# Performance work log

Hardware: AMD Instinct MI355X
Metric: run time of the kernel (lower is better)

## Reference

```python
import jax, jax.numpy as jnp
import numpy as np

B, D, H, W, C = 8, 4, 56, 56, 128
HEADS = 4
WD, WH, WW = 2, 7, 7
SD, SH, SW = 1, 3, 3
N = WD * WH * WW            # tokens per window = 98
NW = (D // WD) * (H // WH) * (W // WW)  # windows per sample = 128
SCALE = (C // HEADS) ** -0.5
EPS = 1e-5


def _rel_pos_index():
    coords = np.stack(np.meshgrid(np.arange(WD), np.arange(WH), np.arange(WW), indexing='ij'))
    coords = coords.reshape(3, -1)                    # (3, N)
    rel = (coords[:, :, None] - coords[:, None, :]).transpose(1, 2, 0)  # (N, N, 3)
    rel[:, :, 0] += WD - 1
    rel[:, :, 1] += WH - 1
    rel[:, :, 2] += WW - 1
    rel[:, :, 0] *= (2 * WH - 1) * (2 * WW - 1)
    rel[:, :, 1] *= (2 * WW - 1)
    return rel.sum(-1)                                # (N, N) int

REL_IDX = jnp.asarray(_rel_pos_index())


def _np_window_partition(x, wd, wh, ww):
    b, d, h, w, c = x.shape
    x = x.reshape(b, d // wd, wd, h // wh, wh, w // ww, ww, c)
    return x.transpose(0, 1, 3, 5, 2, 4, 6, 7).reshape(-1, wd * wh * ww, c)


def _attn_mask():
    img = np.zeros((1, D, H, W, 1), np.float32)
    cnt = 0
    for ds in (slice(None, -WD), slice(-WD, -SD), slice(-SD, None)):
        for hs in (slice(None, -WH), slice(-WH, -SH), slice(-SH, None)):
            for ws in (slice(None, -WW), slice(-WW, -SW), slice(-SW, None)):
                img[:, ds, hs, ws, :] = cnt
                cnt += 1
    mw = _np_window_partition(img, WD, WH, WW)[..., 0]         # (nW, N)
    m = mw[:, None, :] - mw[:, :, None]                        # (nW, N, N)
    return jnp.asarray(np.where(m != 0, -100.0, 0.0).astype(np.float32))

ATTN_MASK = _attn_mask()  # (nW, N, N)


def window_partition(x):
    b = x.shape[0]
    x = x.reshape(b, D // WD, WD, H // WH, WH, W // WW, WW, C)
    return x.transpose(0, 1, 3, 5, 2, 4, 6, 7).reshape(-1, N, C)


def window_reverse(wins, b):
    x = wins.reshape(b, D // WD, H // WH, W // WW, WD, WH, WW, C)
    return x.transpose(0, 1, 4, 2, 5, 3, 6, 7).reshape(b, D, H, W, C)


def layernorm(x, g, b):
    mu = jnp.mean(x, axis=-1, keepdims=True)
    var = jnp.mean(jnp.square(x - mu), axis=-1, keepdims=True)
    return (x - mu) / jnp.sqrt(var + EPS) * g + b


def swin_block(x, norm1_g, norm1_b, qkv_w, qkv_b, rpb_table, proj_w, proj_b,
               norm2_g, norm2_b, fc1_w, fc1_b, fc2_w, fc2_b):
    shortcut = x
    h1 = layernorm(x, norm1_g, norm1_b)
    # cyclic shift (pad amounts are 0 for these dims)
    shifted = jnp.roll(h1, (-SD, -SH, -SW), axis=(1, 2, 3))
    xw = window_partition(shifted)                    # (B*nW, N, C)
    Bn = xw.shape[0]
    qkv = (xw @ qkv_w + qkv_b).reshape(Bn, N, 3, HEADS, C // HEADS)
    qkv = qkv.transpose(2, 0, 3, 1, 4)                # (3, Bn, h, N, c)
    q, k, v = qkv[0], qkv[1], qkv[2]
    attn = jnp.einsum('bhnc,bhmc->bhnm', q * SCALE, k)
    bias = rpb_table[REL_IDX].transpose(2, 0, 1)      # (h, N, N)
    attn = attn + bias[None]
    attn = attn.reshape(B, NW, HEADS, N, N) + ATTN_MASK[None, :, None]
    attn = jax.nn.softmax(attn.reshape(Bn, HEADS, N, N), axis=-1)
    out = jnp.einsum('bhnm,bhmc->bhnc', attn, v)
    out = out.transpose(0, 2, 1, 3).reshape(Bn, N, C)
    out = out @ proj_w + proj_b
    xr = window_reverse(out, B)
    xr = jnp.roll(xr, (SD, SH, SW), axis=(1, 2, 3))
    x1 = shortcut + xr
    h2 = layernorm(x1, norm2_g, norm2_b)
    mlp = jax.nn.gelu(h2 @ fc1_w + fc1_b, approximate=False) @ fc2_w + fc2_b
    return x1 + mlp


def setup_inputs() -> dict:
    key = jax.random.key(0)
    ks = jax.random.split(key, 6)
    s = 0.02
    return {
        'x': jax.random.normal(ks[0], (B, D, H, W, C), jnp.float32),
        'norm1_g': jnp.ones((C,), jnp.float32),
        'norm1_b': jnp.zeros((C,), jnp.float32),
        'qkv_w': jax.random.normal(ks[1], (C, 3 * C), jnp.float32) * s,
        'qkv_b': jnp.zeros((3 * C,), jnp.float32),
        'rpb_table': jax.random.normal(ks[2], ((2 * WD - 1) * (2 * WH - 1) * (2 * WW - 1), HEADS), jnp.float32) * s,
        'proj_w': jax.random.normal(ks[3], (C, C), jnp.float32) * s,
        'proj_b': jnp.zeros((C,), jnp.float32),
        'norm2_g': jnp.ones((C,), jnp.float32),
        'norm2_b': jnp.zeros((C,), jnp.float32),
        'fc1_w': jax.random.normal(ks[4], (C, 4 * C), jnp.float32) * s,
        'fc1_b': jnp.zeros((4 * C,), jnp.float32),
        'fc2_w': jax.random.normal(ks[5], (4 * C, C), jnp.float32) * s,
        'fc2_b': jnp.zeros((C,), jnp.float32),
    }


def reference(x, norm1_g, norm1_b, qkv_w, qkv_b, rpb_table, proj_w, proj_b,
              norm2_g, norm2_b, fc1_w, fc1_b, fc2_w, fc2_b):
    return swin_block(x, norm1_g, norm1_b, qkv_w, qkv_b, rpb_table, proj_w, proj_b,
                      norm2_g, norm2_b, fc1_w, fc1_b, fc2_w, fc2_b)
```

## Files before the change

### kernel.cpp

```cpp
#include <hip/hip_runtime.h>
#include <hip/hip_bf16.h>
#include <cstdint>
#include <cstddef>

using bf16 = __hip_bfloat16;
typedef __bf16 bf16x8 __attribute__((ext_vector_type(8)));
typedef float f32x4 __attribute__((ext_vector_type(4)));

#define DEV static __device__ __forceinline__

DEV bf16 f2b(float x) { return __float2bfloat16(x); }
DEV f32x4 mfma16(bf16x8 a, bf16x8 b, f32x4 c) {
    return __builtin_amdgcn_mfma_f32_16x16x32_bf16(a, b, c, 0, 0, 0);
}
DEV float gelu_f(float x) {
    float u2 = x * x;
    float u = x * (0.7978845608028654f + 0.0356774081363001f * u2);
    float s = 1.f / (1.f + __expf(-2.f * u));
    return x * s;
}
DEV void gload16(const bf16* g, bf16* l) {
    __builtin_amdgcn_global_load_lds(
        (const __attribute__((address_space(1))) unsigned int*)g,
        (__attribute__((address_space(3))) unsigned int*)l, 16, 0, 0);
}

constexpr int NTOK = 98;
constexpr int BNWIN = 1024;
constexpr int MTOT = BNWIN * NTOK;
constexpr float SCALE = 0.17677669529663687f;
constexpr float EPS = 1e-5f;

__global__ __launch_bounds__(256) void k_prep(const float* __restrict__ qkv_w,
        const float* __restrict__ proj_w, const float* __restrict__ fc1_w,
        const float* __restrict__ fc2_w, const float* __restrict__ rpb,
        bf16* __restrict__ QW, bf16* __restrict__ PW,
        bf16* __restrict__ W1, bf16* __restrict__ W2, float* __restrict__ BT) {
    int tid = blockIdx.x * 256 + threadIdx.x;
    int stride = gridDim.x * 256;
    for (int i = tid; i < 384 * 128; i += stride) {
        int n = i >> 7, k = i & 127;
        QW[i] = f2b(qkv_w[k * 384 + n]);
    }
    for (int i = tid; i < 128 * 128; i += stride) {
        int n = i >> 7, k = i & 127;
        PW[i] = f2b(proj_w[k * 128 + n]);
    }
    for (int i = tid; i < 512 * 128; i += stride) {
        int t = i >> 13, r = (i >> 7) & 63, kswz = i & 127;
        int k = kswz ^ ((r & 7) << 3);
        W1[i] = f2b(fc1_w[(size_t)k * 512 + t * 64 + r]);
    }
    for (int i = tid; i < 512 * 128; i += stride) {
        int t = i >> 13, c = (i >> 6) & 127, kswz = i & 63;
        int kk = kswz ^ ((c & 7) << 3);
        W2[i] = f2b(fc2_w[(size_t)(t * 64 + kk) * 128 + c]);
    }
    for (int i = tid; i < 4 * 98 * 98; i += stride) {
        int h = i / 9604, r = i - h * 9604;
        int ii = r / 98, jj = r - ii * 98;
        int di = ii >= 49, ri = ii - di * 49, hi = ri / 7, wi = ri - hi * 7;
        int dj = jj >= 49, rj = jj - dj * 49, hj = rj / 7, wj = rj - hj * 7;
        int bidx = (di - dj + 1) * 169 + (hi - hj + 6) * 13 + (wi - wj + 6);
        BT[i] = rpb[bidx * 4 + h];
    }
}

__global__ __launch_bounds__(256) void k_ln1(const float* __restrict__ x,
        const float* __restrict__ g, const float* __restrict__ be,
        bf16* __restrict__ xw) {
    int wave = threadIdx.x >> 6, lane = threadIdx.x & 63;
    int r = blockIdx.x * 4 + wave;
    int bn = r / 98, n = r - bn * 98;
    int b = bn >> 7, wr = bn & 127;
    int dB = wr >> 6, hB = (wr >> 3) & 7, wB = wr & 7;
    int dd = (n >= 49), rem = n - dd * 49;
    int hh = rem / 7, ww = rem - hh * 7;
    int dp = dB * 2 + dd, hp = hB * 7 + hh, wp = wB * 7 + ww;
    int ds = (dp + 1) & 3;
    int hs = hp + 3; if (hs >= 56) hs -= 56;
    int wsv = wp + 3; if (wsv >= 56) wsv -= 56;
    size_t src = ((size_t)((b * 4 + ds) * 56 + hs) * 56 + wsv) * 128;

    float2 v = *(const float2*)&x[src + lane * 2];
    float v0 = v.x, v1 = v.y;
    float s = v0 + v1, sq = v0 * v0 + v1 * v1;
    #pragma unroll
    for (int m = 1; m < 64; m <<= 1) { s += __shfl_xor(s, m); sq += __shfl_xor(sq, m); }
    float mean = s * (1.f / 128.f);
    float var = sq * (1.f / 128.f) - mean * mean;
    float rstd = rsqrtf(var + EPS);
    float g0 = g[lane * 2], g1 = g[lane * 2 + 1];
    float e0 = be[lane * 2], e1 = be[lane * 2 + 1];
    union { uint32_t u32; bf16 h[2]; } o;
    o.h[0] = f2b((v0 - mean) * rstd * g0 + e0);
    o.h[1] = f2b((v1 - mean) * rstd * g1 + e1);
    *(uint32_t*)&xw[(size_t)r * 128 + lane * 2] = o.u32;
}

__global__ __launch_bounds__(256) void k_qkv(const bf16* __restrict__ A,
        const bf16* __restrict__ QW, const float* __restrict__ bias,
        bf16* __restrict__ out) {
    __shared__ __align__(16) bf16 As[64 * 136];
    __shared__ __align__(16) bf16 Bt[64 * 136];
    int tid = threadIdx.x;
    int row0 = blockIdx.x * 64;
    int col0 = blockIdx.y * 64;
    #pragma unroll
    for (int p = 0; p < 4; ++p) {
        int vi = tid + p * 256;
        int row = vi >> 4, cg = vi & 15;
        *(uint4*)&As[row * 136 + cg * 8] =
            *(const uint4*)&A[(size_t)(row0 + row) * 128 + cg * 8];
    }
    #pragma unroll
    for (int p = 0; p < 4; ++p) {
        int vi = tid + p * 256;
        int row = vi >> 4, cg = vi & 15;
        *(uint4*)&Bt[row * 136 + cg * 8] =
            *(const uint4*)&QW[(size_t)(col0 + row) * 128 + cg * 8];
    }
    __syncthreads();
    int wave = tid >> 6, lane = tid & 63;
    int wr = (wave >> 1) * 32, wc = (wave & 1) * 32;
    int lrow = lane & 15, kg8 = (lane >> 4) * 8, g4 = (lane >> 4) * 4;
    f32x4 acc[2][2] = {};
    #pragma unroll
    for (int ksi = 0; ksi < 4; ++ksi) {
        bf16x8 a[2], bb[2];
        #pragma unroll
        for (int t = 0; t < 2; ++t)
            a[t] = *(const bf16x8*)&As[(wr + t * 16 + lrow) * 136 + ksi * 32 + kg8];
        #pragma unroll
        for (int u2 = 0; u2 < 2; ++u2)
            bb[u2] = *(const bf16x8*)&Bt[(wc + u2 * 16 + lrow) * 136 + ksi * 32 + kg8];
        #pragma unroll
        for (int t = 0; t < 2; ++t)
            #pragma unroll
            for (int u2 = 0; u2 < 2; ++u2)
                acc[t][u2] = mfma16(a[t], bb[u2], acc[t][u2]);
    }
    #pragma unroll
    for (int t = 0; t < 2; ++t)
        #pragma unroll
        for (int u2 = 0; u2 < 2; ++u2) {
            int gcol = col0 + wc + u2 * 16 + lrow;
            float bv = bias[gcol];
            #pragma unroll
            for (int r2 = 0; r2 < 4; ++r2) {
                int grow = row0 + wr + t * 16 + g4 + r2;
                out[(size_t)grow * 384 + gcol] = f2b(acc[t][u2][r2] + bv);
            }
        }
}

__global__ __launch_bounds__(256) void k_attn(const bf16* __restrict__ qkv,
        const float* __restrict__ BT, bf16* __restrict__ aout) {
    __shared__ __align__(16) bf16 qs[112 * 40];
    __shared__ __align__(16) bf16 ksm[112 * 40];
    __shared__ __align__(16) bf16 vt[32 * 136];
    __shared__ __align__(16) bf16 ps[64 * 136];
    __shared__ signed char trg[112];

    int tid = threadIdx.x;
    int bn = blockIdx.x, h = blockIdx.y;
    int wrw = bn & 127;
    int dB = wrw >> 6, hB = (wrw >> 3) & 7, wB = wrw & 7;

    {
        uint32_t* z1 = (uint32_t*)qs;
        uint32_t* z2 = (uint32_t*)ksm;
        for (int i = tid; i < 2240; i += 256) { z1[i] = 0u; z2[i] = 0u; }
        uint32_t* z3 = (uint32_t*)vt;
        for (int i = tid; i < 2176; i += 256) z3[i] = 0u;
        uint32_t* z4 = (uint32_t*)ps;
        for (int i = tid; i < 4352; i += 256) z4[i] = 0u;
    }
    if (tid < 112) {
        int n = tid < 98 ? tid : 97;
        int dd = n >= 49, rem = n - dd * 49;
        int hh = rem / 7, ww2 = rem - hh * 7;
        int dp = dB * 2 + dd, hp = hB * 7 + hh, wp = wB * 7 + ww2;
        int rd = dp < 2 ? 0 : (dp == 2 ? 1 : 2);
        int rh = hp < 49 ? 0 : (hp < 53 ? 1 : 2);
        int rw = wp < 49 ? 0 : (wp < 53 ? 1 : 2);
        trg[tid] = (signed char)(rd * 9 + rh * 3 + rw);
    }
    __syncthreads();
    const size_t base = (size_t)bn * 98 * 384 + h * 32;
    for (int ch = tid; ch < 1176; ch += 256) {
        int mat = ch / 392;
        int rem = ch - mat * 392;
        int row = rem >> 2, cg = rem & 3;
        uint4 v = *(const uint4*)&qkv[base + (size_t)row * 384 + mat * 128 + cg * 8];
        if (mat == 0)      *(uint4*)&qs[row * 40 + cg * 8] = v;
        else if (mat == 1) *(uint4*)&ksm[row * 40 + cg * 8] = v;
        else {
            const bf16* pv = (const bf16*)&v;
            #pragma unroll
            for (int j = 0; j < 8; ++j) vt[(cg * 8 + j) * 136 + row] = pv[j];
        }
    }
    __syncthreads();

    int wave = tid >> 6, lane = tid & 63;
    int lrow = lane & 15, kg8 = (lane >> 4) * 8, g4 = (lane >> 4) * 4;

    for (int rt = wave; rt < 7; rt += 4) {
        f32x4 sacc[7];
        bf16x8 qa = *(const bf16x8*)&qs[(rt * 16 + lrow) * 40 + kg8];
        #pragma unroll
        for (int ct = 0; ct < 7; ++ct) {
            bf16x8 kb = *(const bf16x8*)&ksm[(ct * 16 + lrow) * 40 + kg8];
            f32x4 z = {};
            sacc[ct] = mfma16(qa, kb, z);
        }
        #pragma unroll
        for (int r2 = 0; r2 < 4; ++r2) {
            int grow = rt * 16 + g4 + r2;
            int mi = grow < 98 ? grow : 97;
            int mrg = trg[mi];
            const float* btrow = &BT[((size_t)h * 98 + mi) * 98];
            float val[7];
            float mx = -1e30f;
            #pragma unroll
            for (int ct = 0; ct < 7; ++ct) {
                int jc = ct * 16 + lrow;
                int jj = jc < 98 ? jc : 97;
                float bias = btrow[jj];
                float mv = (mrg != (int)trg[jj]) ? -100.f : 0.f;
                float v = sacc[ct][r2] * SCALE + bias + mv;
                if (jc >= 98) v = -1e30f;
                val[ct] = v;
                mx = fmaxf(mx, v);
            }
            #pragma unroll
            for (int m = 1; m < 16; m <<= 1) mx = fmaxf(mx, __shfl_xor(mx, m));
            float sum = 0.f;
            #pragma unroll
            for (int ct = 0; ct < 7; ++ct) { val[ct] = __expf(val[ct] - mx); sum += val[ct]; }
            #pragma unroll
            for (int m = 1; m < 16; m <<= 1) sum += __shfl_xor(sum, m);
            float inv = 1.f / sum;
            #pragma unroll
            for (int ct = 0; ct < 7; ++ct)
                ps[(wave * 16 + g4 + r2) * 136 + ct * 16 + lrow] = f2b(val[ct] * inv);
        }
        #pragma unroll
        for (int ct = 0; ct < 2; ++ct) {
            f32x4 oacc = {};
            #pragma unroll
            for (int ksi = 0; ksi < 4; ++ksi) {
                bf16x8 pa = *(const bf16x8*)&ps[(wave * 16 + lrow) * 136 + ksi * 32 + kg8];
                bf16x8 vb = *(const bf16x8*)&vt[(ct * 16 + lrow) * 136 + ksi * 32 + kg8];
                oacc = mfma16(pa, vb, oacc);
            }
            #pragma unroll
            for (int r2 = 0; r2 < 4; ++r2) {
                int grow = rt * 16 + g4 + r2;
                if (grow < 98)
                    aout[((size_t)bn * 98 + grow) * 128 + h * 32 + ct * 16 + lrow] =
                        f2b(oacc[r2]);
            }
        }
    }
}

__global__ __launch_bounds__(256) void k_proj(const bf16* __restrict__ A,
        const bf16* __restrict__ PW, const float* __restrict__ pb,
        const float* __restrict__ x, const float* __restrict__ g2,
        const float* __restrict__ be2,
        float* __restrict__ x1, bf16* __restrict__ h2) {
    __shared__ __align__(16) bf16 As[64 * 136];
    __shared__ __align__(16) bf16 Bt[128 * 136];
    int tid = threadIdx.x;
    int row0 = blockIdx.x * 64;
    #pragma unroll
    for (int p = 0; p < 4; ++p) {
        int vi = tid + p * 256;
        int row = vi >> 4, cg = vi & 15;
        *(uint4*)&As[row * 136 + cg * 8] =
            *(const uint4*)&A[(size_t)(row0 + row) * 128 + cg * 8];
    }
    #pragma unroll
    for (int p = 0; p < 8; ++p) {
        int vi = tid + p * 256;
        int row = vi >> 4, cg = vi & 15;
        *(uint4*)&Bt[row * 136 + cg * 8] =
            *(const uint4*)&PW[(size_t)row * 128 + cg * 8];
    }
    __syncthreads();
    int wave = tid >> 6, lane = tid & 63;
    int lrow = lane & 15, kg8 = (lane >> 4) * 8, g4 = (lane >> 4) * 4;
    f32x4 acc[8] = {};
    #pragma unroll
    for (int ksi = 0; ksi < 4; ++ksi) {
        bf16x8 a = *(const bf16x8*)&As[(wave * 16 + lrow) * 136 + ksi * 32 + kg8];
        #pragma unroll
        for (int ct = 0; ct < 8; ++ct) {
            bf16x8 bb = *(const bf16x8*)&Bt[(ct * 16 + lrow) * 136 + ksi * 32 + kg8];
            acc[ct] = mfma16(a, bb, acc[ct]);
        }
    }
    #pragma unroll
    for (int r2 = 0; r2 < 4; ++r2) {
        int rwin = row0 + wave * 16 + g4 + r2;
        int bn = rwin / 98, n = rwin - bn * 98;
        int b = bn >> 7, wr2 = bn & 127;
        int dB = wr2 >> 6, hB = (wr2 >> 3) & 7, wB = wr2 & 7;
        int dd = n >= 49, rem = n - dd * 49;
        int hh = rem / 7, ww2 = rem - hh * 7;
        int dp = dB * 2 + dd, hp = hB * 7 + hh, wp = wB * 7 + ww2;
        int d2 = (dp + 1) & 3;
        int hv = hp + 3; if (hv >= 56) hv -= 56;
        int wv = wp + 3; if (wv >= 56) wv -= 56;
        size_t dst = ((size_t)(b * 4 + d2) * 56 + hv) * 56 + wv;
        float vals[8], s = 0.f, sq = 0.f;
        #pragma unroll
        for (int ct = 0; ct < 8; ++ct) {
            int col = ct * 16 + lrow;
            float v = acc[ct][r2] + pb[col] + x[dst * 128 + col];
            vals[ct] = v; s += v; sq += v * v;
        }
        #pragma unroll
        for (int m = 1; m < 16; m <<= 1) { s += __shfl_xor(s, m); sq += __shfl_xor(sq, m); }
        float mean = s * (1.f / 128.f);
        float var = sq * (1.f / 128.f) - mean * mean;
        float rstd = rsqrtf(var + EPS);
        #pragma unroll
        for (int ct = 0; ct < 8; ++ct) {
            int col = ct * 16 + lrow;
            x1[dst * 128 + col] = vals[ct];
            h2[dst * 128 + col] = f2b((vals[ct] - mean) * rstd * g2[col] + be2[col]);
        }
    }
}

__global__ __launch_bounds__(512) void k_mlp(const bf16* __restrict__ h2,
        const bf16* __restrict__ W1s, const float* __restrict__ b1,
        const bf16* __restrict__ W2s, const float* __restrict__ b2v,
        const float* __restrict__ x1, float* __restrict__ out) {
    __shared__ __align__(16) bf16 W1b[8192];
    __shared__ __align__(16) bf16 W2b[8192];
    __shared__ __align__(16) bf16 Ts[128 * 72];
    int tid = threadIdx.x;
    int row0 = blockIdx.x * 128;
    int wave = tid >> 6, lane = tid & 63;
    int lrow = lane & 15, kg8 = (lane >> 4) * 8, g4 = (lane >> 4) * 4;
    int swz = (lrow & 7) << 3;

    bf16x8 a1[4];
    const bf16* arow = &h2[(size_t)(row0 + wave * 16 + lrow) * 128];
    #pragma unroll
    for (int ksi = 0; ksi < 4; ++ksi)
        a1[ksi] = *(const bf16x8*)&arow[ksi * 32 + kg8];

    f32x4 oacc[8] = {};
    for (int hc = 0; hc < 8; ++hc) {
        const bf16* W1g = W1s + hc * 8192;
        const bf16* W2g = W2s + hc * 8192;
        #pragma unroll
        for (int j = 0; j < 4; ++j) {
            int chunk = wave + j * 8;
            if (chunk < 16) gload16(W1g + chunk * 512 + lane * 8, W1b + chunk * 512);
            else            gload16(W2g + (chunk - 16) * 512 + lane * 8, W2b + (chunk - 16) * 512);
        }
        __syncthreads();

        f32x4 tacc[4] = {};
        #pragma unroll
        for (int ksi = 0; ksi < 4; ++ksi) {
            int k0 = ksi * 32 + kg8;
            #pragma unroll
            for (int ct = 0; ct < 4; ++ct) {
                bf16x8 bb = *(const bf16x8*)&W1b[(ct * 16 + lrow) * 128 + (k0 ^ swz)];
                tacc[ct] = mfma16(a1[ksi], bb, tacc[ct]);
            }
        }
        #pragma unroll
        for (int ct = 0; ct < 4; ++ct) {
            int hcol = hc * 64 + ct * 16 + lrow;
            float bb = b1[hcol];
            #pragma unroll
            for (int r2 = 0; r2 < 4; ++r2) {
                float t = gelu_f(tacc[ct][r2] + bb);
                Ts[(wave * 16 + g4 + r2) * 72 + ct * 16 + lrow] = f2b(t);
            }
        }
        #pragma unroll
        for (int ksi = 0; ksi < 2; ++ksi) {
            int k0 = ksi * 32 + kg8;
            bf16x8 a = *(const bf16x8*)&Ts[(wave * 16 + lrow) * 72 + k0];
            #pragma unroll
            for (int ct = 0; ct < 8; ++ct) {
                bf16x8 bb = *(const bf16x8*)&W2b[(ct * 16 + lrow) * 64 + (k0 ^ swz)];
                oacc[ct] = mfma16(a, bb, oacc[ct]);
            }
        }
        __syncthreads();
    }
    #pragma unroll
    for (int ct = 0; ct < 8; ++ct) {
        int col = ct * 16 + lrow;
        float bb = b2v[col];
        #pragma unroll
        for (int r2 = 0; r2 < 4; ++r2) {
            size_t grow = (size_t)row0 + wave * 16 + g4 + r2;
            out[grow * 128 + col] = oacc[ct][r2] + bb + x1[grow * 128 + col];
        }
    }
}

extern "C" void kernel_launch(void* const* d_in, const int* in_sizes, int n_in,
                              void* d_out, int out_size, void* d_ws, size_t ws_size,
                              hipStream_t stream) {
    (void)in_sizes; (void)n_in; (void)out_size; (void)ws_size;
    const float* x      = (const float*)d_in[0];
    const float* n1g    = (const float*)d_in[1];
    const float* n1b    = (const float*)d_in[2];
    const float* qkv_w  = (const float*)d_in[3];
    const float* qkv_b  = (const float*)d_in[4];
    const float* rpb    = (const float*)d_in[5];
    const float* proj_w = (const float*)d_in[6];
    const float* proj_b = (const float*)d_in[7];
    const float* n2g    = (const float*)d_in[8];
    const float* n2b    = (const float*)d_in[9];
    const float* fc1_w  = (const float*)d_in[10];
    const float* fc1_b  = (const float*)d_in[11];
    const float* fc2_w  = (const float*)d_in[12];
    const float* fc2_b  = (const float*)d_in[13];
    float* outp = (float*)d_out;

    char* ws = (char*)d_ws;
    constexpr size_t S = (size_t)MTOT * 128 * 2;
    bf16*  xw     = (bf16*)ws;
    bf16*  qkvbuf = (bf16*)(ws + S);
    bf16*  aout   = xw;
    float* x1     = (float*)(ws + S);
    bf16*  h2     = (bf16*)(ws + 3 * S);
    char* wp_ = ws + 4 * S;
    bf16*  QW  = (bf16*)wp_;
    bf16*  PW  = (bf16*)(wp_ + 98304);
    bf16*  W1s = (bf16*)(wp_ + 98304 + 32768);
    bf16*  W2s = (bf16*)(wp_ + 98304 + 32768 + 131072);
    float* BTb = (float*)(wp_ + 98304 + 32768 + 131072 + 131072);

    k_prep<<<192, 256, 0, stream>>>(qkv_w, proj_w, fc1_w, fc2_w, rpb, QW, PW, W1s, W2s, BTb);
    k_ln1 <<<MTOT / 4, 256, 0, stream>>>(x, n1g, n1b, xw);
    k_qkv <<<dim3(MTOT / 64, 6), 256, 0, stream>>>(xw, QW, qkv_b, qkvbuf);
    k_attn<<<dim3(BNWIN, 4), 256, 0, stream>>>(qkvbuf, BTb, aout);
    k_proj<<<MTOT / 64, 256, 0, stream>>>(aout, PW, proj_b, x, n2g, n2b, x1, h2);
    k_mlp <<<MTOT / 128, 512, 0, stream>>>(h2, W1s, fc1_b, W2s, fc2_b, x1, outp);
}
```

Baseline: 221.7 us.

## Fuse LayerNorm1 into QKV GEMM and store residual x1 in bf16

Merges the LayerNorm kernel into the QKV projection: each block normalizes its 64 gathered, shifted rows directly into shared memory and loops over all six column tiles, streaming pre-swizzled weight tiles via direct global-to-LDS loads. This removes the intermediate normalized-activation buffer write/read and the repeated activation reloads across six column blocks. Separately, the post-attention residual x1 is stored in bf16 instead of fp32, halving its traffic at the cost of residual precision. The fused kernel uses fewer blocks and serializes column tiles within a block.

```diff
diff --git a/kernel.cpp b/kernel.cpp
--- a/kernel.cpp
+++ b/kernel.cpp
@@ -10,6 +10,7 @@
 #define DEV static __device__ __forceinline__
 
 DEV bf16 f2b(float x) { return __float2bfloat16(x); }
+DEV float b2f(bf16 x) { return __bfloat162float(x); }
 DEV f32x4 mfma16(bf16x8 a, bf16x8 b, f32x4 c) {
     return __builtin_amdgcn_mfma_f32_16x16x32_bf16(a, b, c, 0, 0, 0);
 }
@@ -34,13 +35,14 @@
 __global__ __launch_bounds__(256) void k_prep(const float* __restrict__ qkv_w,
         const float* __restrict__ proj_w, const float* __restrict__ fc1_w,
         const float* __restrict__ fc2_w, const float* __restrict__ rpb,
-        bf16* __restrict__ QW, bf16* __restrict__ PW,
+        bf16* __restrict__ QWs, bf16* __restrict__ PW,
         bf16* __restrict__ W1, bf16* __restrict__ W2, float* __restrict__ BT) {
     int tid = blockIdx.x * 256 + threadIdx.x;
     int stride = gridDim.x * 256;
     for (int i = tid; i < 384 * 128; i += stride) {
-        int n = i >> 7, k = i & 127;
-        QW[i] = f2b(qkv_w[k * 384 + n]);
+        int t = i >> 13, r = (i >> 7) & 63, kswz = i & 127;
+        int k = kswz ^ ((r & 7) << 3);
+        QWs[i] = f2b(qkv_w[(size_t)k * 384 + t * 64 + r]);
     }
     for (int i = tid; i < 128 * 128; i += stride) {
         int n = i >> 7, k = i & 127;
@@ -66,92 +68,94 @@
     }
 }
 
-__global__ __launch_bounds__(256) void k_ln1(const float* __restrict__ x,
+__global__ __launch_bounds__(256) void k_qkvln(const float* __restrict__ x,
         const float* __restrict__ g, const float* __restrict__ be,
-        bf16* __restrict__ xw) {
-    int wave = threadIdx.x >> 6, lane = threadIdx.x & 63;
-    int r = blockIdx.x * 4 + wave;
-    int bn = r / 98, n = r - bn * 98;
-    int b = bn >> 7, wr = bn & 127;
-    int dB = wr >> 6, hB = (wr >> 3) & 7, wB = wr & 7;
-    int dd = (n >= 49), rem = n - dd * 49;
-    int hh = rem / 7, ww = rem - hh * 7;
-    int dp = dB * 2 + dd, hp = hB * 7 + hh, wp = wB * 7 + ww;
-    int ds = (dp + 1) & 3;
-    int hs = hp + 3; if (hs >= 56) hs -= 56;
-    int wsv = wp + 3; if (wsv >= 56) wsv -= 56;
-    size_t src = ((size_t)((b * 4 + ds) * 56 + hs) * 56 + wsv) * 128;
-
-    float2 v = *(const float2*)&x[src + lane * 2];
-    float v0 = v.x, v1 = v.y;
-    float s = v0 + v1, sq = v0 * v0 + v1 * v1;
-    #pragma unroll
-    for (int m = 1; m < 64; m <<= 1) { s += __shfl_xor(s, m); sq += __shfl_xor(sq, m); }
-    float mean = s * (1.f / 128.f);
-    float var = sq * (1.f / 128.f) - mean * mean;
-    float rstd = rsqrtf(var + EPS);
-    float g0 = g[lane * 2], g1 = g[lane * 2 + 1];
-    float e0 = be[lane * 2], e1 = be[lane * 2 + 1];
-    union { uint32_t u32; bf16 h[2]; } o;
-    o.h[0] = f2b((v0 - mean) * rstd * g0 + e0);
-    o.h[1] = f2b((v1 - mean) * rstd * g1 + e1);
-    *(uint32_t*)&xw[(size_t)r * 128 + lane * 2] = o.u32;
-}
-
-__global__ __launch_bounds__(256) void k_qkv(const bf16* __restrict__ A,
-        const bf16* __restrict__ QW, const float* __restrict__ bias,
+        const bf16* __restrict__ QWs, const float* __restrict__ bias,
         bf16* __restrict__ out) {
     __shared__ __align__(16) bf16 As[64 * 136];
-    __shared__ __align__(16) bf16 Bt[64 * 136];
+    __shared__ __align__(16) bf16 Bt[64 * 128];
     int tid = threadIdx.x;
     int row0 = blockIdx.x * 64;
-    int col0 = blockIdx.y * 64;
+    int wave = tid >> 6, lane = tid & 63;
+    int lrow = lane & 15, kg8 = (lane >> 4) * 8, g4 = (lane >> 4) * 4;
+    int swzq = (lrow & 7) << 3;
+
     #pragma unroll
     for (int p = 0; p < 4; ++p) {
         int vi = tid + p * 256;
         int row = vi >> 4, cg = vi & 15;
-        *(uint4*)&As[row * 136 + cg * 8] =
-            *(const uint4*)&A[(size_t)(row0 + row) * 128 + cg * 8];
-    }
-    #pragma unroll
-    for (int p = 0; p < 4; ++p) {
-        int vi = tid + p * 256;
-        int row = vi >> 4, cg = vi & 15;
-        *(uint4*)&Bt[row * 136 + cg * 8] =
-            *(const uint4*)&QW[(size_t)(col0 + row) * 128 + cg * 8];
+        int r = row0 + row;
+        int bn = r / 98, n = r - bn * 98;
+        int b = bn >> 7, wr = bn & 127;
+        int dB = wr >> 6, hB = (wr >> 3) & 7, wB = wr & 7;
+        int dd = (n >= 49), rem = n - dd * 49;
+        int hh = rem / 7, ww = rem - hh * 7;
+        int dp = dB * 2 + dd, hp = hB * 7 + hh, wp = wB * 7 + ww;
+        int ds = (dp + 1) & 3;
+        int hs = hp + 3; if (hs >= 56) hs -= 56;
+        int wsv = wp + 3; if (wsv >= 56) wsv -= 56;
+        size_t src = ((size_t)((b * 4 + ds) * 56 + hs) * 56 + wsv) * 128 + cg * 8;
+        float4 v0 = *(const float4*)&x[src];
+        float4 v1 = *(const float4*)&x[src + 4];
+        float s = v0.x + v0.y + v0.z + v0.w + v1.x + v1.y + v1.z + v1.w;
+        float sq = v0.x*v0.x + v0.y*v0.y + v0.z*v0.z + v0.w*v0.w
+                 + v1.x*v1.x + v1.y*v1.y + v1.z*v1.z + v1.w*v1.w;
+        #pragma unroll
+        for (int m = 1; m < 16; m <<= 1) { s += __shfl_xor(s, m); sq += __shfl_xor(sq, m); }
+        float mean = s * (1.f / 128.f);
+        float var = sq * (1.f / 128.f) - mean * mean;
+        float rstd = rsqrtf(var + EPS);
+        float4 g0 = *(const float4*)&g[cg * 8], g1 = *(const float4*)&g[cg * 8 + 4];
+        float4 e0 = *(const float4*)&be[cg * 8], e1 = *(const float4*)&be[cg * 8 + 4];
+        union { bf16x8 v8; bf16 h[8]; } o;
+        o.h[0] = f2b((v0.x - mean) * rstd * g0.x + e0.x);
+        o.h[1] = f2b((v0.y - mean) * rstd * g0.y + e0.y);
+        o.h[2] = f2b((v0.z - mean) * rstd * g0.z + e0.z);
+        o.h[3] = f2b((v0.w - mean) * rstd * g0.w + e0.w);
+        o.h[4] = f2b((v1.x - mean) * rstd * g1.x + e1.x);
+        o.h[5] = f2b((v1.y - mean) * rstd * g1.y + e1.y);
+        o.h[6] = f2b((v1.z - mean) * rstd * g1.z + e1.z);
+        o.h[7] = f2b((v1.w - mean) * rstd * g1.w + e1.w);
+        *(bf16x8*)&As[row * 136 + cg * 8] = o.v8;
     }
     __syncthreads();
-    int wave = tid >> 6, lane = tid & 63;
-    int wr = (wave >> 1) * 32, wc = (wave & 1) * 32;
-    int lrow = lane & 15, kg8 = (lane >> 4) * 8, g4 = (lane >> 4) * 4;
-    f32x4 acc[2][2] = {};
-    #pragma unroll
-    for (int ksi = 0; ksi < 4; ++ksi) {
-        bf16x8 a[2], bb[2];
-        #pragma unroll
-        for (int t = 0; t < 2; ++t)
-            a[t] = *(const bf16x8*)&As[(wr + t * 16 + lrow) * 136 + ksi * 32 + kg8];
-        #pragma unroll
-        for (int u2 = 0; u2 < 2; ++u2)
-            bb[u2] = *(const bf16x8*)&Bt[(wc + u2 * 16 + lrow) * 136 + ksi * 32 + kg8];
-        #pragma unroll
-        for (int t = 0; t < 2; ++t)
-            #pragma unroll
-            for (int u2 = 0; u2 < 2; ++u2)
-                acc[t][u2] = mfma16(a[t], bb[u2], acc[t][u2]);
-    }
-    #pragma unroll
-    for (int t = 0; t < 2; ++t)
-        #pragma unroll
-        for (int u2 = 0; u2 < 2; ++u2) {
-            int gcol = col0 + wc + u2 * 16 + lrow;
+
+    bf16x8 a1[4];
+    #pragma unroll
+    for (int ksi = 0; ksi < 4; ++ksi)
+        a1[ksi] = *(const bf16x8*)&As[(wave * 16 + lrow) * 136 + ksi * 32 + kg8];
+
+    for (int c6 = 0; c6 < 6; ++c6) {
+        const bf16* Bg = QWs + c6 * 8192;
+        #pragma unroll
+        for (int j = 0; j < 4; ++j) {
+            int chunk = wave * 4 + j;
+            gload16(Bg + chunk * 512 + lane * 8, Bt + chunk * 512);
+        }
+        __syncthreads();
+
+        f32x4 acc[4] = {};
+        #pragma unroll
+        for (int ksi = 0; ksi < 4; ++ksi) {
+            int k0 = ksi * 32 + kg8;
+            #pragma unroll
+            for (int ct = 0; ct < 4; ++ct) {
+                bf16x8 bb = *(const bf16x8*)&Bt[(ct * 16 + lrow) * 128 + (k0 ^ swzq)];
+                acc[ct] = mfma16(a1[ksi], bb, acc[ct]);
+            }
+        }
+        #pragma unroll
+        for (int ct = 0; ct < 4; ++ct) {
+            int gcol = c6 * 64 + ct * 16 + lrow;
             float bv = bias[gcol];
             #pragma unroll
             for (int r2 = 0; r2 < 4; ++r2) {
-                int grow = row0 + wr + t * 16 + g4 + r2;
-                out[(size_t)grow * 384 + gcol] = f2b(acc[t][u2][r2] + bv);
-            }
-        }
+                int grow = row0 + wave * 16 + g4 + r2;
+                out[(size_t)grow * 384 + gcol] = f2b(acc[ct][r2] + bv);
+            }
+        }
+        __syncthreads();
+    }
 }
 
 __global__ __launch_bounds__(256) void k_attn(const bf16* __restrict__ qkv,
@@ -270,7 +274,7 @@
         const bf16* __restrict__ PW, const float* __restrict__ pb,
         const float* __restrict__ x, const float* __restrict__ g2,
         const float* __restrict__ be2,
-        float* __restrict__ x1, bf16* __restrict__ h2) {
+        bf16* __restrict__ x1, bf16* __restrict__ h2) {
     __shared__ __align__(16) bf16 As[64 * 136];
     __shared__ __align__(16) bf16 Bt[128 * 136];
     int tid = threadIdx.x;
@@ -330,7 +334,7 @@
         #pragma unroll
         for (int ct = 0; ct < 8; ++ct) {
             int col = ct * 16 + lrow;
-            x1[dst * 128 + col] = vals[ct];
+            x1[dst * 128 + col] = f2b(vals[ct]);
             h2[dst * 128 + col] = f2b((vals[ct] - mean) * rstd * g2[col] + be2[col]);
         }
     }
@@ -339,7 +343,7 @@
 __global__ __launch_bounds__(512) void k_mlp(const bf16* __restrict__ h2,
         const bf16* __restrict__ W1s, const float* __restrict__ b1,
         const bf16* __restrict__ W2s, const float* __restrict__ b2v,
-        const float* __restrict__ x1, float* __restrict__ out) {
+        const bf16* __restrict__ x1, float* __restrict__ out) {
     __shared__ __align__(16) bf16 W1b[8192];
     __shared__ __align__(16) bf16 W2b[8192];
     __shared__ __align__(16) bf16 Ts[128 * 72];
@@ -406,7 +410,7 @@
         #pragma unroll
         for (int r2 = 0; r2 < 4; ++r2) {
             size_t grow = (size_t)row0 + wave * 16 + g4 + r2;
-            out[grow * 128 + col] = oacc[ct][r2] + bb + x1[grow * 128 + col];
+            out[grow * 128 + col] = oacc[ct][r2] + bb + b2f(x1[grow * 128 + col]);
         }
     }
 }
@@ -433,22 +437,20 @@
 
     char* ws = (char*)d_ws;
     constexpr size_t S = (size_t)MTOT * 128 * 2;
-    bf16*  xw     = (bf16*)ws;
     bf16*  qkvbuf = (bf16*)(ws + S);
-    bf16*  aout   = xw;
-    float* x1     = (float*)(ws + S);
+    bf16*  aout   = (bf16*)ws;
+    bf16*  x1     = (bf16*)(ws + S);
     bf16*  h2     = (bf16*)(ws + 3 * S);
     char* wp_ = ws + 4 * S;
-    bf16*  QW  = (bf16*)wp_;
+    bf16*  QWs = (bf16*)wp_;
     bf16*  PW  = (bf16*)(wp_ + 98304);
     bf16*  W1s = (bf16*)(wp_ + 98304 + 32768);
     bf16*  W2s = (bf16*)(wp_ + 98304 + 32768 + 131072);
     float* BTb = (float*)(wp_ + 98304 + 32768 + 131072 + 131072);
 
-    k_prep<<<192, 256, 0, stream>>>(qkv_w, proj_w, fc1_w, fc2_w, rpb, QW, PW, W1s, W2s, BTb);
-    k_ln1 <<<MTOT / 4, 256, 0, stream>>>(x, n1g, n1b, xw);
-    k_qkv <<<dim3(MTOT / 64, 6), 256, 0, stream>>>(xw, QW, qkv_b, qkvbuf);
-    k_attn<<<dim3(BNWIN, 4), 256, 0, stream>>>(qkvbuf, BTb, aout);
-    k_proj<<<MTOT / 64, 256, 0, stream>>>(aout, PW, proj_b, x, n2g, n2b, x1, h2);
-    k_mlp <<<MTOT / 128, 512, 0, stream>>>(h2, W1s, fc1_b, W2s, fc2_b, x1, outp);
-}
+    k_prep <<<192, 256, 0, stream>>>(qkv_w, proj_w, fc1_w, fc2_w, rpb, QWs, PW, W1s, W2s, BTb);
+    k_qkvln<<<MTOT / 64, 256, 0, stream>>>(x, n1g, n1b, QWs, qkv_b, qkvbuf);
+    k_attn <<<dim3(BNWIN, 4), 256, 0, stream>>>(qkvbuf, BTb, aout);
+    k_proj <<<MTOT / 64, 256, 0, stream>>>(aout, PW, proj_b, x, n2g, n2b, x1, h2);
+    k_mlp  <<<MTOT / 128, 512, 0, stream>>>(h2, W1s, fc1_b, W2s, fc2_b, x1, outp);
+}
```

After: 197.6 us (median of 2 runs). 10.9% less time.
